# Optimization experiments

Measured on AMD Instinct MI355X. Metric: run time of the kernel, lower is better.

## Reference

```python
import jax, jax.numpy as jnp
import numpy as np

TOP_K = 4  # top_k_neighbors from __init__


def setup_inputs() -> dict:
    key = jax.random.key(0)
    k1, k2, k3, k4 = jax.random.split(key, 4)
    R, B, D, N = 256, 64, 512, 16
    h = jax.random.normal(k1, (R, B, D), dtype=jnp.float32)
    nbrs = jax.random.randint(k2, (R, N), 0, R, dtype=jnp.int32)
    W_msg = jax.random.normal(k3, (D, D), dtype=jnp.float32) * 0.02
    b_msg = jnp.zeros((D,), dtype=jnp.float32)
    W_merge = jax.random.normal(k4, (D, 2 * D), dtype=jnp.float32) * 0.02
    b_merge = jnp.zeros((D,), dtype=jnp.float32)
    return {
        "h_by_region": h,
        "neighbor_indices": nbrs,
        "W_msg": W_msg,
        "b_msg": b_msg,
        "W_merge": W_merge,
        "b_merge": b_merge,
    }


def reference(h_by_region, neighbor_indices, W_msg, b_msg, W_merge, b_merge):
    # h_by_region: [R, B, D]; neighbor_indices: [R, N] int32
    R, B, D = h_by_region.shape
    h = h_by_region
    # sim(r, j) = mean over (B, D) of h[r] * h[j]. Compute the full Gram once
    # ([R, R], tiny) instead of materializing [R, N, B, D] just for sims.
    G = jnp.einsum('rbd,sbd->rs', h, h) / (B * D)
    sims = jnp.take_along_axis(G, neighbor_indices, axis=1)           # [R, N]
    _, top = jax.lax.top_k(sims, TOP_K)                               # [R, K]
    sel = jnp.take_along_axis(neighbor_indices, top, axis=1)          # [R, K]
    # Gather selected neighbor states, project to messages, average over K.
    h_sel = h[sel]                                                    # [R, K, B, D]
    msgs = jnp.einsum('rkbd,ed->rkbe', h_sel, W_msg) + b_msg          # [R, K, B, D]
    m = msgs.mean(axis=1)                                             # [R, B, D]
    cat = jnp.concatenate([h, m], axis=-1)                            # [R, B, 2D]
    out = jnp.einsum('rbf,ef->rbe', cat, W_merge) + b_merge           # [R, B, D]
    avg_fanin = jnp.float32(TOP_K)  # every region keeps exactly top_k neighbors
    return out, avg_fanin
```

## Files before the change

### kernel.cpp

```cpp
#include <hip/hip_runtime.h>
#include <hip/hip_bf16.h>

#define R_ 256
#define B_ 64
#define D_ 512
#define N_ 16
#define K_ 4
#define RBD (B_ * D_)
#define OUT_ELEMS (R_ * B_ * D_)
#define M_TOT (R_ * B_)
#define GSLICES 64

typedef __attribute__((address_space(1))) unsigned int g_u32;
typedef __attribute__((address_space(3))) unsigned int l_u32;
using f32x4 = __attribute__((ext_vector_type(4))) float;
using f16x8 = __attribute__((ext_vector_type(8))) _Float16;
using f16x4 = __attribute__((ext_vector_type(4))) _Float16;

__global__ __launch_bounds__(256, 4) void gramx_kernel(
    const float* __restrict__ h, const float* __restrict__ Wm,
    const float* __restrict__ Wmsg, _Float16* __restrict__ A16,
    float* __restrict__ Cp, float* __restrict__ W2p) {
  __shared__ char smem[32768];
  const int t = threadIdx.x;
  const int bid = blockIdx.x;

  if (bid >= 1024) {
    const int gid = bid - 1024;
    const int db = (gid & 15) * 32;
    const int eb = ((gid >> 4) & 15) * 32;
    const int kc = gid >> 8;
    float(*As)[33] = (float(*)[33])smem;
    float(*Bs)[33] = (float(*)[33])(smem + 32 * 33 * 4);
    const int tx = t % 16, ty = t / 16;
    const int lr = t / 8;
    const int lc = (t % 8) * 4;
    float a00 = 0.f, a01 = 0.f, a10 = 0.f, a11 = 0.f;
    for (int c0 = kc * 128; c0 < kc * 128 + 128; c0 += 32) {
      float4 av = *(const float4*)&Wm[(size_t)(eb + lr) * 1024 + 512 + c0 + lc];
      float4 bv = *(const float4*)&Wmsg[(size_t)(c0 + lr) * 512 + db + lc];
      As[lr][lc + 0] = av.x; As[lr][lc + 1] = av.y;
      As[lr][lc + 2] = av.z; As[lr][lc + 3] = av.w;
      Bs[lr][lc + 0] = bv.x; Bs[lr][lc + 1] = bv.y;
      Bs[lr][lc + 2] = bv.z; Bs[lr][lc + 3] = bv.w;
      __syncthreads();
#pragma unroll
      for (int kk = 0; kk < 32; kk++) {
        float x0 = As[2 * ty + 0][kk], x1 = As[2 * ty + 1][kk];
        float y0 = Bs[kk][2 * tx + 0], y1 = Bs[kk][2 * tx + 1];
        a00 += x0 * y0; a01 += x0 * y1;
        a10 += x1 * y0; a11 += x1 * y1;
      }
      __syncthreads();
    }
    float* base = W2p + (size_t)kc * 512 * 512;
    base[(size_t)(eb + 2 * ty + 0) * 512 + db + 2 * tx + 0] = a00;
    base[(size_t)(eb + 2 * ty + 0) * 512 + db + 2 * tx + 1] = a01;
    base[(size_t)(eb + 2 * ty + 1) * 512 + db + 2 * tx + 0] = a10;
    base[(size_t)(eb + 2 * ty + 1) * 512 + db + 2 * tx + 1] = a11;
    return;
  }

  const int work = (bid & 7) * 128 + (bid >> 3);
  const int s = work >> 4;
  const int bx = work & 3;
  const int by = (work >> 2) & 3;
  const int I = bx * 64;
  const int J = by * 64;
  const bool duty = (bx == by);
  const int lane = t & 63;
  const int w = t >> 6;
  char* sHiI = smem;
  char* sHiJ = smem + 8192;
  char* sLoJ = smem + 16384;
  char* sLoI = smem + 24576;
  const int wm = w >> 1, wn = w & 1;
  const int rlane = lane & 15;
  const int kq = lane >> 4;

  f32x4 c1[2][2] = {};
  f32x4 c2[2][2] = {};
  f32x4 c3[2][2] = {};

  const float* hI = h + (size_t)I * RBD + (size_t)s * 512;
  const float* hJ = h + (size_t)J * RBD + (size_t)s * 512;
  const int frow = t >> 4;
  const int fc4 = t & 15;

  float4 rI[4], rJ[4];
#pragma unroll
  for (int u = 0; u < 4; ++u) {
    const int row = u * 16 + frow;
    rI[u] = *(const float4*)&hI[(size_t)row * RBD + fc4 * 4];
    rJ[u] = *(const float4*)&hJ[(size_t)row * RBD + fc4 * 4];
  }

  for (int kt = 0; kt < 8; ++kt) {
    if (kt) __syncthreads();
#pragma unroll
    for (int u = 0; u < 4; ++u) {
      const int row = u * 16 + frow;
      const int boff =
          row * 128 + (((fc4 >> 1) ^ (row & 7)) << 4) + (fc4 & 1) * 8;
      float4 vI = rI[u];
      f16x4 hiI = {(_Float16)vI.x, (_Float16)vI.y, (_Float16)vI.z,
                   (_Float16)vI.w};
      f16x4 loI = {(_Float16)(vI.x - (float)hiI[0]),
                   (_Float16)(vI.y - (float)hiI[1]),
                   (_Float16)(vI.z - (float)hiI[2]),
                   (_Float16)(vI.w - (float)hiI[3])};
      *(f16x4*)(sHiI + boff) = hiI;
      *(f16x4*)(sLoI + boff) = loI;
      float4 vJ = rJ[u];
      f16x4 hiJ = {(_Float16)vJ.x, (_Float16)vJ.y, (_Float16)vJ.z,
                   (_Float16)vJ.w};
      f16x4 loJ = {(_Float16)(vJ.x - (float)hiJ[0]),
                   (_Float16)(vJ.y - (float)hiJ[1]),
                   (_Float16)(vJ.z - (float)hiJ[2]),
                   (_Float16)(vJ.w - (float)hiJ[3])};
      *(f16x4*)(sHiJ + boff) = hiJ;
      *(f16x4*)(sLoJ + boff) = loJ;
      if (duty)
        *(f16x4*)&A16[(size_t)(J + row) * RBD + (size_t)s * 512 + kt * 64 +
                      fc4 * 4] = hiJ;
    }
    __syncthreads();
    if (kt < 7) {
#pragma unroll
      for (int u = 0; u < 4; ++u) {
        const int row = u * 16 + frow;
        rI[u] =
            *(const float4*)&hI[(size_t)row * RBD + (kt + 1) * 64 + fc4 * 4];
        rJ[u] =
            *(const float4*)&hJ[(size_t)row * RBD + (kt + 1) * 64 + fc4 * 4];
      }
    }
#pragma unroll
    for (int ks = 0; ks < 2; ++ks) {
      f16x8 ai[2], li[2], bj[2], lj[2];
#pragma unroll
      for (int i = 0; i < 2; ++i) {
        const int row = wm * 32 + i * 16 + rlane;
        const int slot = (ks * 4 + kq) ^ (row & 7);
        ai[i] = *(const f16x8*)(sHiI + row * 128 + slot * 16);
        li[i] = *(const f16x8*)(sLoI + row * 128 + slot * 16);
      }
#pragma unroll
      for (int j = 0; j < 2; ++j) {
        const int row = wn * 32 + j * 16 + rlane;
        const int slot = (ks * 4 + kq) ^ (row & 7);
        bj[j] = *(const f16x8*)(sHiJ + row * 128 + slot * 16);
        lj[j] = *(const f16x8*)(sLoJ + row * 128 + slot * 16);
      }
#pragma unroll
      for (int i = 0; i < 2; ++i)
#pragma unroll
        for (int j = 0; j < 2; ++j) {
          c1[i][j] = __builtin_amdgcn_mfma_f32_16x16x32_f16(ai[i], bj[j],
                                                            c1[i][j], 0, 0, 0);
          c2[i][j] = __builtin_amdgcn_mfma_f32_16x16x32_f16(ai[i], lj[j],
                                                            c2[i][j], 0, 0, 0);
          c3[i][j] = __builtin_amdgcn_mfma_f32_16x16x32_f16(li[i], bj[j],
                                                            c3[i][j], 0, 0, 0);
        }
    }
  }

#pragma unroll
  for (int i = 0; i < 2; ++i) {
#pragma unroll
    for (int reg = 0; reg < 4; ++reg) {
      const int gr = I + wm * 32 + i * 16 + kq * 4 + reg;
      const size_t base = ((size_t)s * 256 + gr) * 256 + J + wn * 32 + rlane;
#pragma unroll
      for (int j = 0; j < 2; ++j)
        Cp[base + j * 16] =
            c1[i][j][reg] + c2[i][j][reg] + c3[i][j][reg];
    }
  }
}

__global__ __launch_bounds__(256) void fin_kernel(
    const float* __restrict__ Cp, const int* __restrict__ nbrs,
    const float* __restrict__ W2p, const float* __restrict__ Wm,
    const float* __restrict__ b_msg, const float* __restrict__ b_merge,
    int* __restrict__ sel, float* __restrict__ fanin,
    _Float16* __restrict__ W16, float* __restrict__ bias_eff) {
  const int bx = blockIdx.x;
  const int t = threadIdx.x;
  if (bx < 256) {
    const int r = bx;
    __shared__ float sims_all[256];
    __shared__ int nb_s[N_];
    const float* base = Cp + (size_t)r * 256 + t;
    float acc = 0.f;
#pragma unroll 8
    for (int s = 0; s < GSLICES; ++s) acc += base[(size_t)s * 65536];
    sims_all[t] = acc;
    if (t < N_) nb_s[t] = nbrs[r * N_ + t];
    __syncthreads();
    if (t == 0) {
      float sims_s[N_];
#pragma unroll
      for (int n = 0; n < N_; ++n) sims_s[n] = sims_all[nb_s[n]];
      unsigned used = 0;
#pragma unroll
      for (int k = 0; k < K_; k++) {
        float best = -3.0e38f;
        int bi = 0;
        for (int nn = 0; nn < N_; nn++) {
          if (used & (1u << nn)) continue;
          float vv = sims_s[nn];
          if (vv > best) { best = vv; bi = nn; }
        }
        used |= 1u << bi;
        sel[r * K_ + k] = nb_s[bi];
      }
      if (r == 0) *fanin = 4.0f;
    }
  } else if (bx < 1280) {
    const int i = (bx - 256) * 256 + t;
    const int e = i >> 9;
    const int d = i & 511;
    float acc = 0.f;
#pragma unroll
    for (int kc = 0; kc < 4; ++kc)
      acc += W2p[(size_t)kc * 512 * 512 + (size_t)e * 512 + d];
    W16[(size_t)e * 1024 + 512 + d] = (_Float16)acc;
  } else if (bx < 1536) {
    const int i = (bx - 1280) * 256 + t;
    const int e = i >> 7;
    const int c4 = (i & 127) * 4;
    float4 v = *(const float4*)&Wm[(size_t)e * 1024 + c4];
    f16x4 o = {(_Float16)v.x, (_Float16)v.y, (_Float16)v.z, (_Float16)v.w};
    *(f16x4*)&W16[(size_t)e * 1024 + c4] = o;
  } else {
    const int e = (bx - 1536) * 256 + t;
    const float4* bp = (const float4*)b_msg;
    const float4* wp = (const float4*)&Wm[(size_t)e * 1024 + 512];
    float acc = 0.f;
    for (int c = 0; c < 128; c++) {
      float4 b4 = bp[c], w4 = wp[c];
      acc += b4.x * w4.x + b4.y * w4.y + b4.z * w4.z + b4.w * w4.w;
    }
    bias_eff[e] = acc + b_merge[e];
  }
}

__global__ __launch_bounds__(256, 4) void mfma_gemm_kernel(
    const _Float16* __restrict__ A16, const int* __restrict__ sel,
    const _Float16* __restrict__ W16, const float* __restrict__ bias,
    float* __restrict__ out) {
  const int t = threadIdx.x;
  const int lane = t & 63;
  const int w = t >> 6;
  const int bid = blockIdx.x;
  const int work = (bid & 7) * 128 + (bid >> 3);
  const int eb = (work & 3) * 128;
  const int my = work >> 2;
  const int m0 = my * 64;
  __shared__ char smemA[64 * 128];
  __shared__ char smemW[128 * 128];
  __shared__ int sel_s[4];
  const int wm = w >> 1, wn = w & 1;
  const int rlane = lane & 15;
  const int kq = lane >> 4;

  if (t < 4) sel_s[t] = sel[my * 4 + t];
  __syncthreads();

  f32x4 acc[2][4] = {};

  const char* Ab = (const char*)A16;
  const char* Wb = (const char*)W16;
  const _Float16* g0 = A16;
  const _Float16* g1;
  const _Float16* g2;
  const _Float16* g3;
  g0 = A16 + (size_t)sel_s[0] * RBD;
  g1 = A16 + (size_t)sel_s[1] * RBD;
  g2 = A16 + (size_t)sel_s[2] * RBD;
  g3 = A16 + (size_t)sel_s[3] * RBD;

  for (int kt = 0; kt < 16; ++kt) {
    if (kt < 8) {
#pragma unroll
      for (int u = 0; u < 2; ++u) {
        const int f = u * 256 + t;
        const int row = f >> 3;
        const int slot = (f & 7) ^ (row & 7);
        const char* ga =
            Ab + ((size_t)(m0 + row) * 1024 + kt * 128 + slot * 16);
        char* la = smemA + u * 4096 + w * 1024;
        __builtin_amdgcn_global_load_lds((const g_u32*)ga, (l_u32*)la, 16, 0,
                                         0);
      }
    } else {
      const int kk8 = kt - 8;
#pragma unroll
      for (int u = 0; u < 2; ++u) {
        const int f = u * 256 + t;
        const int row = f >> 3;
        const int slot = f & 7;
        const size_t off = (size_t)row * 512 + kk8 * 64 + slot * 8;
        f16x8 q0 = *(const f16x8*)&g0[off];
        f16x8 q1 = *(const f16x8*)&g1[off];
        f16x8 q2 = *(const f16x8*)&g2[off];
        f16x8 q3 = *(const f16x8*)&g3[off];
        f16x8 m = ((q0 + q1) + (q2 + q3)) * (_Float16)0.25f;
        *(f16x8*)(smemA + row * 128 + ((slot ^ (row & 7)) << 4)) = m;
      }
    }
#pragma unroll
    for (int q = 0; q < 4; ++q) {
      const int f = q * 256 + t;
      const int row = f >> 3;
      const int slot = (f & 7) ^ (row & 7);
      const char* gw = Wb + ((size_t)(eb + row) * 2048 + kt * 128 + slot * 16);
      char* lw = smemW + q * 4096 + w * 1024;
      __builtin_amdgcn_global_load_lds((const g_u32*)gw, (l_u32*)lw, 16, 0, 0);
    }
    __syncthreads();
#pragma unroll
    for (int ks = 0; ks < 2; ++ks) {
      f16x8 a[2], b[4];
#pragma unroll
      for (int i = 0; i < 2; ++i) {
        const int row = wm * 32 + i * 16 + rlane;
        const int slot = (ks * 4 + kq) ^ (row & 7);
        a[i] = *(const f16x8*)(smemA + row * 128 + slot * 16);
      }
#pragma unroll
      for (int j = 0; j < 4; ++j) {
        const int row = wn * 64 + j * 16 + rlane;
        const int slot = (ks * 4 + kq) ^ (row & 7);
        b[j] = *(const f16x8*)(smemW + row * 128 + slot * 16);
      }
#pragma unroll
      for (int i = 0; i < 2; ++i)
#pragma unroll
        for (int j = 0; j < 4; ++j)
          acc[i][j] = __builtin_amdgcn_mfma_f32_16x16x32_f16(a[i], b[j],
                                                             acc[i][j], 0, 0, 0);
    }
    __syncthreads();
  }

  float bj[4];
#pragma unroll
  for (int j = 0; j < 4; ++j) bj[j] = bias[eb + wn * 64 + j * 16 + rlane];
#pragma unroll
  for (int i = 0; i < 2; ++i) {
#pragma unroll
    for (int reg = 0; reg < 4; ++reg) {
      const size_t m = (size_t)m0 + wm * 32 + i * 16 + kq * 4 + reg;
      float* po = out + m * 512 + eb + wn * 64 + rlane;
#pragma unroll
      for (int j = 0; j < 4; ++j) po[j * 16] = acc[i][j][reg] + bj[j];
    }
  }
}

__global__ __launch_bounds__(256) void bias_kernel(
    const float* __restrict__ Wm, const float* __restrict__ b_msg,
    const float* __restrict__ b_merge, float* __restrict__ bias_eff) {
  const int e = blockIdx.x * 256 + threadIdx.x;
  const float4* bp = (const float4*)b_msg;
  const float4* wp = (const float4*)&Wm[(size_t)e * 1024 + 512];
  float acc = 0.f;
  for (int c = 0; c < 128; c++) {
    float4 b4 = bp[c], w4 = wp[c];
    acc += b4.x * w4.x + b4.y * w4.y + b4.z * w4.z + b4.w * w4.w;
  }
  bias_eff[e] = acc + b_merge[e];
}

__global__ __launch_bounds__(256) void sims_topk_kernel(
    const float* __restrict__ h, const int* __restrict__ nbrs,
    int* __restrict__ sel, float* __restrict__ fanin) {
  const int r = blockIdx.x;
  const int t = threadIdx.x;
  const int lane = t & 63;
  const int wave = t >> 6;
  __shared__ float sims_s[N_];
  __shared__ int nb_s[N_];
  if (t < N_) nb_s[t] = nbrs[r * N_ + t];
  __syncthreads();
  const int n0 = wave * 4;
  const float4* hr  = (const float4*)(h + (size_t)r * RBD);
  const float4* hn0 = (const float4*)(h + (size_t)nb_s[n0 + 0] * RBD);
  const float4* hn1 = (const float4*)(h + (size_t)nb_s[n0 + 1] * RBD);
  const float4* hn2 = (const float4*)(h + (size_t)nb_s[n0 + 2] * RBD);
  const float4* hn3 = (const float4*)(h + (size_t)nb_s[n0 + 3] * RBD);
  float a0 = 0.f, a1 = 0.f, a2 = 0.f, a3 = 0.f;
  for (int i = lane; i < RBD / 4; i += 64) {
    float4 x = hr[i];
    float4 y0 = hn0[i], y1 = hn1[i], y2 = hn2[i], y3 = hn3[i];
    a0 += x.x * y0.x + x.y * y0.y + x.z * y0.z + x.w * y0.w;
    a1 += x.x * y1.x + x.y * y1.y + x.z * y1.z + x.w * y1.w;
    a2 += x.x * y2.x + x.y * y2.y + x.z * y2.z + x.w * y2.w;
    a3 += x.x * y3.x + x.y * y3.y + x.z * y3.z + x.w * y3.w;
  }
  float v[4] = {a0, a1, a2, a3};
#pragma unroll
  for (int n = 0; n < 4; n++) {
    float x = v[n];
#pragma unroll
    for (int off = 32; off > 0; off >>= 1) x += __shfl_down(x, off);
    if (lane == 0) sims_s[n0 + n] = x;
  }
  __syncthreads();
  if (t == 0) {
    unsigned used = 0;
#pragma unroll
    for (int k = 0; k < K_; k++) {
      float best = -3.0e38f;
      int bi = 0;
      for (int n = 0; n < N_; n++) {
        if (used & (1u << n)) continue;
        float vv = sims_s[n];
        if (vv > best) { best = vv; bi = n; }
      }
      used |= 1u << bi;
      sel[r * K_ + k] = nb_s[bi];
    }
    if (r == 0) *fanin = 4.0f;
  }
}

__global__ __launch_bounds__(256) void w2eff_f32_kernel(
    const float* __restrict__ Wm, const float* __restrict__ Wmsg,
    float* __restrict__ W2) {
  __shared__ float As[32][33];
  __shared__ float Bs[32][33];
  const int t = threadIdx.x;
  const int eb = blockIdx.y * 32;
  const int db = blockIdx.x * 32;
  const int tx = t % 16, ty = t / 16;
  const int lr = t / 8;
  const int lc = (t % 8) * 4;
  float a00 = 0.f, a01 = 0.f, a10 = 0.f, a11 = 0.f;
  for (int c0 = 0; c0 < 512; c0 += 32) {
    float4 av = *(const float4*)&Wm[(size_t)(eb + lr) * 1024 + 512 + c0 + lc];
    float4 bv = *(const float4*)&Wmsg[(size_t)(c0 + lr) * 512 + db + lc];
    As[lr][lc + 0] = av.x; As[lr][lc + 1] = av.y;
    As[lr][lc + 2] = av.z; As[lr][lc + 3] = av.w;
    Bs[lr][lc + 0] = bv.x; Bs[lr][lc + 1] = bv.y;
    Bs[lr][lc + 2] = bv.z; Bs[lr][lc + 3] = bv.w;
    __syncthreads();
#pragma unroll
    for (int kk = 0; kk < 32; kk++) {
      float x0 = As[2 * ty + 0][kk], x1 = As[2 * ty + 1][kk];
      float y0 = Bs[kk][2 * tx + 0], y1 = Bs[kk][2 * tx + 1];
      a00 += x0 * y0; a01 += x0 * y1;
      a10 += x1 * y0; a11 += x1 * y1;
    }
    __syncthreads();
  }
  W2[(size_t)(eb + 2 * ty + 0) * 512 + db + 2 * tx + 0] = a00;
  W2[(size_t)(eb + 2 * ty + 0) * 512 + db + 2 * tx + 1] = a01;
  W2[(size_t)(eb + 2 * ty + 1) * 512 + db + 2 * tx + 0] = a10;
  W2[(size_t)(eb + 2 * ty + 1) * 512 + db + 2 * tx + 1] = a11;
}

__global__ __launch_bounds__(256) void fused_gemm_f32_kernel(
    const float* __restrict__ h, const int* __restrict__ sel,
    const float* __restrict__ Wm, const float* __restrict__ W2,
    const float* __restrict__ bias_eff, float* __restrict__ out) {
  const int r = blockIdx.y;
  const int eb = blockIdx.x * 256;
  const int t = threadIdx.x;
  __shared__ float As[64][33];
  __shared__ float Ws[256][33];
  __shared__ int sel_s[K_];
  if (t < K_) sel_s[t] = sel[r * K_ + t];
  __syncthreads();
  const size_t hr = (size_t)r * RBD;
  const size_t s0 = (size_t)sel_s[0] * RBD;
  const size_t s1 = (size_t)sel_s[1] * RBD;
  const size_t s2 = (size_t)sel_s[2] * RBD;
  const size_t s3 = (size_t)sel_s[3] * RBD;
  const int tb = t % 8;
  const int te = t / 8;
  const int ab = t / 4;
  const int ac = (t % 4) * 8;
  float acc[8][8] = {};
  for (int d0 = 0; d0 < 1024; d0 += 32) {
    if (d0 < 512) {
      const float* src = h + hr + (size_t)ab * 512 + d0 + ac;
      float4 v0 = *(const float4*)(src);
      float4 v1 = *(const float4*)(src + 4);
      As[ab][ac + 0] = v0.x; As[ab][ac + 1] = v0.y;
      As[ab][ac + 2] = v0.z; As[ab][ac + 3] = v0.w;
      As[ab][ac + 4] = v1.x; As[ab][ac + 5] = v1.y;
      As[ab][ac + 6] = v1.z; As[ab][ac + 7] = v1.w;
    } else {
      const size_t off = (size_t)ab * 512 + (d0 - 512) + ac;
      const float* p0 = h + s0 + off;
      const float* p1 = h + s1 + off;
      const float* p2 = h + s2 + off;
      const float* p3 = h + s3 + off;
      float4 q0 = *(const float4*)p0, q0b = *(const float4*)(p0 + 4);
      float4 q1 = *(const float4*)p1, q1b = *(const float4*)(p1 + 4);
      float4 q2 = *(const float4*)p2, q2b = *(const float4*)(p2 + 4);
      float4 q3 = *(const float4*)p3, q3b = *(const float4*)(p3 + 4);
      As[ab][ac + 0] = 0.25f * (q0.x + q1.x + q2.x + q3.x);
      As[ab][ac + 1] = 0.25f * (q0.y + q1.y + q2.y + q3.y);
      As[ab][ac + 2] = 0.25f * (q0.z + q1.z + q2.z + q3.z);
      As[ab][ac + 3] = 0.25f * (q0.w + q1.w + q2.w + q3.w);
      As[ab][ac + 4] = 0.25f * (q0b.x + q1b.x + q2b.x + q3b.x);
      As[ab][ac + 5] = 0.25f * (q0b.y + q1b.y + q2b.y + q3b.y);
      As[ab][ac + 6] = 0.25f * (q0b.z + q1b.z + q2b.z + q3b.z);
      As[ab][ac + 7] = 0.25f * (q0b.w + q1b.w + q2b.w + q3b.w);
    }
    {
      const float* src = (d0 < 512)
          ? (Wm + (size_t)(eb + t) * 1024 + d0)
          : (W2 + (size_t)(eb + t) * 512 + (d0 - 512));
#pragma unroll
      for (int j = 0; j < 8; j++) {
        float4 v = *(const float4*)(src + 4 * j);
        Ws[t][4 * j + 0] = v.x; Ws[t][4 * j + 1] = v.y;
        Ws[t][4 * j + 2] = v.z; Ws[t][4 * j + 3] = v.w;
      }
    }
    __syncthreads();
#pragma unroll
    for (int kk = 0; kk < 32; kk++) {
      float a[8], wv[8];
#pragma unroll
      for (int i = 0; i < 8; i++) a[i] = As[tb + 8 * i][kk];
#pragma unroll
      for (int j = 0; j < 8; j++) wv[j] = Ws[te + 32 * j][kk];
#pragma unroll
      for (int i = 0; i < 8; i++)
#pragma unroll
        for (int j = 0; j < 8; j++) acc[i][j] += a[i] * wv[j];
    }
    __syncthreads();
  }
  float be[8];
#pragma unroll
  for (int j = 0; j < 8; j++) be[j] = bias_eff[eb + te + 32 * j];
#pragma unroll
  for (int i = 0; i < 8; i++) {
    const int b = tb + 8 * i;
#pragma unroll
    for (int j = 0; j < 8; j++) {
      const int e = eb + te + 32 * j;
      out[hr + (size_t)b * 512 + e] = acc[i][j] + be[j];
    }
  }
}

extern "C" void kernel_launch(void* const* d_in, const int* in_sizes, int n_in,
                              void* d_out, int out_size, void* d_ws,
                              size_t ws_size, hipStream_t stream) {
  const float* h       = (const float*)d_in[0];
  const int*   nbrs    = (const int*)d_in[1];
  const float* W_msg   = (const float*)d_in[2];
  const float* b_msg   = (const float*)d_in[3];
  const float* W_merge = (const float*)d_in[4];
  const float* b_merge = (const float*)d_in[5];
  float* out = (float*)d_out;
  char* ws = (char*)d_ws;

  const size_t SZ_PART = (size_t)GSLICES * 256 * 256 * 4;
  const size_t SZ_A = (size_t)M_TOT * 512 * 2;
  const size_t SZ_W = (size_t)512 * 1024 * 2;
  const size_t SZ_W2P = (size_t)4 * 512 * 512 * 4;
  size_t off = 0;
  int*      sel      = (int*)(ws + off);      off += 4096;
  float*    bias_eff = (float*)(ws + off);    off += 4096;
  float*    Cp       = (float*)(ws + off);    off += SZ_PART;
  _Float16* A16      = (_Float16*)(ws + off); off += SZ_A;
  _Float16* W16      = (_Float16*)(ws + off); off += SZ_W;
  float*    W2p      = (float*)(ws + off);    off += SZ_W2P;
  const size_t NEED = off;

  if (ws_size >= NEED) {
    gramx_kernel<<<2048, 256, 0, stream>>>(h, W_merge, W_msg, A16, Cp, W2p);
    fin_kernel<<<1538, 256, 0, stream>>>(Cp, nbrs, W2p, W_merge, b_msg,
                                         b_merge, sel, out + OUT_ELEMS, W16,
                                         bias_eff);
    mfma_gemm_kernel<<<1024, 256, 0, stream>>>(A16, sel, W16, bias_eff, out);
  } else {
    int*   fsel     = (int*)ws;
    float* W2       = (float*)(ws + 4096);
    float* fbias    = (float*)(ws + 4096 + 512 * 512 * 4);
    sims_topk_kernel<<<R_, 256, 0, stream>>>(h, nbrs, fsel, out + OUT_ELEMS);
    bias_kernel<<<2, 256, 0, stream>>>(W_merge, b_msg, b_merge, fbias);
    w2eff_f32_kernel<<<dim3(16, 16), 256, 0, stream>>>(W_merge, W_msg, W2);
    fused_gemm_f32_kernel<<<dim3(2, R_), 256, 0, stream>>>(h, fsel, W_merge,
                                                           W2, fbias, out);
  }
}
```

Measured before the change: 86.65 us.

## Exploit Gram symmetry: compute only upper-triangular tile pairs and mirror-store

The Gram partial kernel now launches blocks only for the 10 upper-triangular 64x64 tile pairs per slice instead of all 16, and each off-diagonal block also writes its transposed result into the mirrored location of the partial buffer. This removes redundant MFMA work and the associated loads of h for the lower triangle. In exchange it adds a strided transposed store per off-diagonal tile and a constant-memory lookup for the tile pair. A small cleanup of pointer initialisation in the GEMM kernel is included.

```diff
diff --git a/kernel.cpp b/kernel.cpp
--- a/kernel.cpp
+++ b/kernel.cpp
@@ -10,12 +10,17 @@
 #define OUT_ELEMS (R_ * B_ * D_)
 #define M_TOT (R_ * B_)
 #define GSLICES 64
+#define GPAIRS 10
+#define GBLK (GSLICES * GPAIRS)
 
 typedef __attribute__((address_space(1))) unsigned int g_u32;
 typedef __attribute__((address_space(3))) unsigned int l_u32;
 using f32x4 = __attribute__((ext_vector_type(4))) float;
 using f16x8 = __attribute__((ext_vector_type(8))) _Float16;
 using f16x4 = __attribute__((ext_vector_type(4))) _Float16;
+
+__constant__ int kBx[GPAIRS] = {0, 0, 0, 0, 1, 1, 1, 2, 2, 3};
+__constant__ int kBy[GPAIRS] = {0, 1, 2, 3, 1, 2, 3, 2, 3, 3};
 
 __global__ __launch_bounds__(256, 4) void gramx_kernel(
     const float* __restrict__ h, const float* __restrict__ Wm,
@@ -25,8 +30,8 @@
   const int t = threadIdx.x;
   const int bid = blockIdx.x;
 
-  if (bid >= 1024) {
-    const int gid = bid - 1024;
+  if (bid >= GBLK) {
+    const int gid = bid - GBLK;
     const int db = (gid & 15) * 32;
     const int eb = ((gid >> 4) & 15) * 32;
     const int kc = gid >> 8;
@@ -61,10 +66,11 @@
     return;
   }
 
-  const int work = (bid & 7) * 128 + (bid >> 3);
-  const int s = work >> 4;
-  const int bx = work & 3;
-  const int by = (work >> 2) & 3;
+  const int work = (bid & 7) * (GBLK / 8) + (bid >> 3);
+  const int s = work / GPAIRS;
+  const int pr = work % GPAIRS;
+  const int bx = kBx[pr];
+  const int by = kBy[pr];
   const int I = bx * 64;
   const int J = by * 64;
   const bool duty = (bx == by);
@@ -166,6 +172,13 @@
     }
   }
 
+  f32x4 cs[2][2];
+#pragma unroll
+  for (int i = 0; i < 2; ++i)
+#pragma unroll
+    for (int j = 0; j < 2; ++j)
+      cs[i][j] = c1[i][j] + c2[i][j] + c3[i][j];
+
 #pragma unroll
   for (int i = 0; i < 2; ++i) {
 #pragma unroll
@@ -173,10 +186,18 @@
       const int gr = I + wm * 32 + i * 16 + kq * 4 + reg;
       const size_t base = ((size_t)s * 256 + gr) * 256 + J + wn * 32 + rlane;
 #pragma unroll
-      for (int j = 0; j < 2; ++j)
-        Cp[base + j * 16] =
-            c1[i][j][reg] + c2[i][j][reg] + c3[i][j][reg];
-    }
+      for (int j = 0; j < 2; ++j) Cp[base + j * 16] = cs[i][j][reg];
+    }
+  }
+  if (!duty) {
+#pragma unroll
+    for (int i = 0; i < 2; ++i)
+#pragma unroll
+      for (int j = 0; j < 2; ++j) {
+        const int gc = J + wn * 32 + j * 16 + rlane;
+        const int gr0 = I + wm * 32 + i * 16 + kq * 4;
+        *(f32x4*)&Cp[((size_t)s * 256 + gc) * 256 + gr0] = cs[i][j];
+      }
   }
 }
 
@@ -273,14 +294,10 @@
 
   const char* Ab = (const char*)A16;
   const char* Wb = (const char*)W16;
-  const _Float16* g0 = A16;
-  const _Float16* g1;
-  const _Float16* g2;
-  const _Float16* g3;
-  g0 = A16 + (size_t)sel_s[0] * RBD;
-  g1 = A16 + (size_t)sel_s[1] * RBD;
-  g2 = A16 + (size_t)sel_s[2] * RBD;
-  g3 = A16 + (size_t)sel_s[3] * RBD;
+  const _Float16* g0 = A16 + (size_t)sel_s[0] * RBD;
+  const _Float16* g1 = A16 + (size_t)sel_s[1] * RBD;
+  const _Float16* g2 = A16 + (size_t)sel_s[2] * RBD;
+  const _Float16* g3 = A16 + (size_t)sel_s[3] * RBD;
 
   for (int kt = 0; kt < 16; ++kt) {
     if (kt < 8) {
@@ -579,7 +596,8 @@
   const size_t NEED = off;
 
   if (ws_size >= NEED) {
-    gramx_kernel<<<2048, 256, 0, stream>>>(h, W_merge, W_msg, A16, Cp, W2p);
+    gramx_kernel<<<GBLK + 1024, 256, 0, stream>>>(h, W_merge, W_msg, A16, Cp,
+                                                  W2p);
     fin_kernel<<<1538, 256, 0, stream>>>(Cp, nbrs, W2p, W_merge, b_msg,
                                          b_merge, sel, out + OUT_ELEMS, W16,
                                          bias_eff);
```

New measurement: 81.64 us. -5.8%, faster.
